# Optimization experiments

Measured on AMD Instinct MI355X. Metric: run time of the kernel, lower is better.

The kernel has to match this reference:

```python
import jax, jax.numpy as jnp
import numpy as np

B, G, NB, NC = 1024, 28, 2, 20
THR_CONF = 3.0
THR_NMS = 0.3
K = 4096            # fixed top-k detection slots (jit-friendly padding)
NEG = jnp.float32(-1e30)


def setup_inputs() -> dict:
    key = jax.random.key(0)
    k1, k2, k3 = jax.random.split(key, 3)
    return {
        "p_boxes": jax.random.normal(k1, (B, G, G, NB * 4), dtype=jnp.float32),
        "p_confs": jax.random.normal(k2, (B, G, G, NB), dtype=jnp.float32),
        "p_clses": jax.random.normal(k3, (B, G, G, NC), dtype=jnp.float32),
    }


def _decode_topk(p_boxes, p_confs, p_clses):
    # boxes: (B,G,G,NB,4) with (offx, offy, w, h) per box slot
    boxes = p_boxes.reshape(B, G, G, NB, 4)
    col = jnp.arange(G, dtype=jnp.float32)
    row = jnp.arange(G, dtype=jnp.float32)
    # offxy2xy: xy = (offxy + colrow) / num_grid  (dim1=row, dim2=col per torch.where order)
    cx = (boxes[..., 0] + col[None, None, :, None]) / G
    cy = (boxes[..., 1] + row[None, :, None, None]) / G
    w, h = boxes[..., 2], boxes[..., 3]
    # xywh2ltrb
    ltrb = jnp.stack([cx - w * 0.5, cy - h * 0.5, cx + w * 0.5, cy + h * 0.5], axis=-1)
    # label = argmax over classes + 1, shared by both box slots of a cell
    labels = jnp.argmax(p_clses, axis=-1) + 1                       # (B,G,G)
    labels = jnp.broadcast_to(labels[..., None], (B, G, G, NB))
    bids = jnp.broadcast_to(jnp.arange(B)[:, None, None, None], (B, G, G, NB))
    valid = p_confs > THR_CONF

    N = B * G * G * NB
    scores_masked = jnp.where(valid, p_confs, NEG).reshape(N)
    topv, topi = jax.lax.top_k(scores_masked, K)                    # sorted desc
    boxes_k = ltrb.reshape(N, 4)[topi]
    labels_k = labels.reshape(N)[topi]
    bids_k = bids.reshape(N)[topi]
    scores_k = p_confs.reshape(N)[topi]
    valid_k = topv > THR_CONF
    return bids_k, boxes_k, labels_k, scores_k, valid_k


def _iou_matrix(b):
    # b: (K,4) ltrb -> (K,K) pairwise IoU
    lt = jnp.maximum(b[:, None, :2], b[None, :, :2])
    rb = jnp.minimum(b[:, None, 2:], b[None, :, 2:])
    wh = jnp.clip(rb - lt, 0.0)
    inter = wh[..., 0] * wh[..., 1]
    area = jnp.clip(b[:, 2] - b[:, 0], 0.0) * jnp.clip(b[:, 3] - b[:, 1], 0.0)
    union = area[:, None] + area[None, :] - inter
    return inter / jnp.maximum(union, 1e-9)


def _nms(boxes, groups, valid):
    # per-(batch,label) NMS via group equality mask; boxes pre-sorted by score desc
    same = groups[:, None] == groups[None, :]
    suppress = same & (_iou_matrix(boxes) > THR_NMS)                # (K,K)
    idx = jnp.arange(K)

    def body(i, keep):
        sup = jnp.any(keep & suppress[:, i] & (idx < i))
        return keep.at[i].set(valid[i] & ~sup)

    return jax.lax.fori_loop(0, K, body, jnp.zeros((K,), dtype=bool))


def reference(p_boxes, p_confs, p_clses):
    bids, boxes, labels, scores, valid = _decode_topk(p_boxes, p_confs, p_clses)
    groups = bids * (NC + 1) + labels
    keep = _nms(boxes, groups, valid)
    # padded outputs of fixed size K; `keep` marks surviving detections
    return bids, boxes, labels, scores, keep
```

## Files before the change

### kernel.cpp

```cpp
#include <hip/hip_runtime.h>
#include <stdint.h>

#define B_    1024
#define G_    28
#define NB_   2
#define NC_   20
#define KK    4096
#define NTOT  (B_*G_*G_*NB_)
#define THRC  3.0f
#define THRN  0.3f
#define SORT_N 8192
#define NGRP  (B_*(NC_+1))
#define GCAP  8
#define RB    256
#define KPB   64
#define NRBF  (SORT_N/KPB)
#define CPT   16

#define WS_CNT   0
#define WS_GCNT  256
#define WS_ZERO_BYTES (256 + NGRP*4)
#define WS_KEYS  86272
#define WS_GMEM  (WS_KEYS + SORT_N*8)

typedef unsigned long long u64;

__global__ void k_zero(int4* __restrict__ p) {
    int t = blockIdx.x * blockDim.x + threadIdx.x;
    if (t < WS_ZERO_BYTES / 16) p[t] = make_int4(0, 0, 0, 0);
}

__global__ void k_collect(const float4* __restrict__ conf4, const float* __restrict__ clses,
                          u64* __restrict__ keys, int* cnt,
                          int* __restrict__ gcnt, u64* __restrict__ gmem) {
    int t = blockIdx.x * blockDim.x + threadIdx.x;
    int lane = threadIdx.x & 63;
    float cc[CPT];
    #pragma unroll
    for (int q = 0; q < CPT / 4; ++q) {
        float4 v = conf4[t * (CPT / 4) + q];
        cc[q * 4 + 0] = v.x; cc[q * 4 + 1] = v.y;
        cc[q * 4 + 2] = v.z; cc[q * 4 + 3] = v.w;
    }
    int nh = 0;
    #pragma unroll
    for (int u = 0; u < CPT; ++u) nh += (cc[u] > THRC);
    u64 act = __ballot(nh > 0);
    if (act) {
        int incl = nh;
        #pragma unroll
        for (int off = 1; off < 64; off <<= 1) {
            int v = __shfl_up(incl, off);
            if (lane >= off) incl += v;
        }
        int tot = __shfl(incl, 63);
        int base = 0;
        if (lane == 0) base = atomicAdd(cnt, tot);
        base = __shfl(base, 0);
        int pos = base + incl - nh;
        int fb = t * CPT;
        #pragma unroll
        for (int u = 0; u < CPT; ++u) {
            if (cc[u] > THRC) {
                int idx = fb + u;
                unsigned b = __float_as_uint(cc[u]);
                b = (b & 0x80000000u) ? ~b : (b | 0x80000000u);
                u64 key = ((u64)b << 32) | (u64)(0xFFFFFFFFu - (unsigned)idx);
                if (pos < SORT_N) keys[pos] = key;
                pos++;
                int cell = idx >> 1;
                const float4* cp4 = (const float4*)(clses + (size_t)cell * NC_);
                float best = -3.4e38f; int lab = 0;
                #pragma unroll
                for (int q = 0; q < 5; ++q) {
                    float4 cv = cp4[q];
                    float vv[4] = {cv.x, cv.y, cv.z, cv.w};
                    #pragma unroll
                    for (int w = 0; w < 4; ++w) {
                        int ci = q * 4 + w;
                        if (vv[w] > best) { best = vv[w]; lab = ci; }
                    }
                }
                int g = (cell / (G_ * G_)) * (NC_ + 1) + (lab + 1);
                int p2 = atomicAdd(&gcnt[g], 1);
                if (p2 < GCAP) gmem[(size_t)g * GCAP + p2] = key;
            }
        }
    }
}

__device__ inline float4 box_of(int idx, const float* __restrict__ boxes) {
    int nb = idx & 1;
    int cell = idx >> 1;
    int gx = cell % G_;
    int gy = (cell / G_) % G_;
    float4 bv = *(const float4*)(boxes + (size_t)cell * (NB_ * 4) + nb * 4);
    float cx = (bv.x + (float)gx) / (float)G_;
    float cy = (bv.y + (float)gy) / (float)G_;
    return make_float4(cx - bv.z * 0.5f, cy - bv.w * 0.5f,
                       cx + bv.z * 0.5f, cy + bv.w * 0.5f);
}

struct Dec { int b; int lab; };
__device__ inline Dec decode_write(int slot, int idx, float score,
                                   const float* __restrict__ boxes,
                                   const float* __restrict__ clses,
                                   float* __restrict__ out) {
    int cell = idx >> 1;
    int b = cell / (G_ * G_);
    float4 lt = box_of(idx, boxes);
    const float4* cp4 = (const float4*)(clses + (size_t)cell * NC_);
    float best = -3.4e38f; int lab = 0;
    #pragma unroll
    for (int q = 0; q < 5; ++q) {
        float4 cv = cp4[q];
        float vv[4] = {cv.x, cv.y, cv.z, cv.w};
        #pragma unroll
        for (int u = 0; u < 4; ++u) {
            int ci = q * 4 + u;
            if (vv[u] > best) { best = vv[u]; lab = ci; }
        }
    }
    lab += 1;
    out[slot] = (float)b;
    *(float4*)(out + KK + 4*slot) = lt;
    out[5*KK + slot] = (float)lab;
    out[6*KK + slot] = score;
    out[7*KK + slot] = 0.0f;
    Dec d; d.b = b; d.lab = lab;
    return d;
}

__global__ void __launch_bounds__(RB) k_rankdec(const float* __restrict__ boxes,
                                                const float4* __restrict__ conf4,
                                                const float* __restrict__ conf,
                                                const float* __restrict__ clses,
                                                const int* __restrict__ cnt,
                                                const u64* __restrict__ keys,
                                                float* __restrict__ out,
                                                const int* __restrict__ gcnt,
                                                const u64* __restrict__ gmem) {
    int tid = threadIdx.x;
    int lane = tid & 63;
    int Vtot = min(cnt[0], SORT_N);
    int V = min(Vtot, KK);

    if (blockIdx.x == NRBF) {
        __shared__ int wsum[4];
        int M = KK - V;
        if (M <= 0) return;
        unsigned mask = 0;
        int base = tid * 32;
        #pragma unroll
        for (int q = 0; q < 8; ++q) {
            float4 cv = conf4[tid * 8 + q];
            mask |= (unsigned)(!(cv.x > THRC)) << (q * 4 + 0);
            mask |= (unsigned)(!(cv.y > THRC)) << (q * 4 + 1);
            mask |= (unsigned)(!(cv.z > THRC)) << (q * 4 + 2);
            mask |= (unsigned)(!(cv.w > THRC)) << (q * 4 + 3);
        }
        int c = __popc(mask);
        int incl = c;
        #pragma unroll
        for (int off = 1; off < 64; off <<= 1) {
            int v = __shfl_up(incl, off);
            if (lane >= off) incl += v;
        }
        int wid = tid >> 6;
        if (lane == 63) wsum[wid] = incl;
        __syncthreads();
        int wbase = 0;
        for (int w = 0; w < wid; ++w) wbase += wsum[w];
        int p = wbase + incl - c;
        unsigned m = mask;
        while (m) {
            int u = __builtin_ctz(m);
            if (p < M) {
                int idx = base + u;
                decode_write(V + p, idx, conf[idx], boxes, clses, out);
            }
            p++;
            m &= m - 1;
        }
        return;
    }

    __shared__ u64 sk[SORT_N];
    __shared__ int partial[KPB][5];
    if (blockIdx.x * KPB >= Vtot) return;
    const ulonglong2* keys2 = (const ulonglong2*)keys;
    for (int i = tid; i * 2 < Vtot; i += RB) {
        ulonglong2 kv = keys2[i];
        sk[2 * i]     = kv.x;
        sk[2 * i + 1] = kv.y;
    }
    __syncthreads();

    int k = tid & (KPB - 1);
    int q = tid >> 6;
    int t = blockIdx.x * KPB + k;
    int chunk = (Vtot + 3) >> 2;
    int j0 = q * chunk;
    int j1 = min(j0 + chunk, Vtot);
    int r4 = 0;
    if (t < Vtot) {
        u64 k0 = sk[t];
        int j = j0;
        int lim = j0 + ((j1 - j0) & ~7);
        for (; j < lim; j += 8) {
            r4 += (int)(sk[j+0] > k0) + (int)(sk[j+1] > k0)
                + (int)(sk[j+2] > k0) + (int)(sk[j+3] > k0)
                + (int)(sk[j+4] > k0) + (int)(sk[j+5] > k0)
                + (int)(sk[j+6] > k0) + (int)(sk[j+7] > k0);
        }
        for (; j < j1; ++j) r4 += (int)(sk[j] > k0);
    }
    partial[k][q] = r4;
    __syncthreads();

    if (tid >= KPB || t >= Vtot) return;
    int r = partial[tid][0] + partial[tid][1] + partial[tid][2] + partial[tid][3];
    if (r >= KK) return;
    u64 k0 = sk[t];
    int idx = (int)(0xFFFFFFFFu - (unsigned)(k0 & 0xFFFFFFFFull));
    float score = __uint_as_float((unsigned)(k0 >> 32) ^ 0x80000000u);
    Dec d = decode_write(r, idx, score, boxes, clses, out);

    int g = d.b * (NC_ + 1) + d.lab;
    int m = min(gcnt[g], GCAP);
    u64 mem[GCAP];
    for (int i = 0; i < m; ++i) mem[i] = gmem[(size_t)g * GCAP + i];
    for (int i = 1; i < m; ++i) {
        u64 v = mem[i]; int qq = i - 1;
        while (qq >= 0 && mem[qq] < v) { mem[qq + 1] = mem[qq]; --qq; }
        mem[qq + 1] = v;
    }
    bool survive;
    if (m <= 1) {
        survive = true;
    } else {
        int own = 0;
        float4 bx[GCAP]; float ar[GCAP];
        for (int i = 0; i < m; ++i) {
            if (mem[i] == k0) own = i;
            int mi = (int)(0xFFFFFFFFu - (unsigned)(mem[i] & 0xFFFFFFFFull));
            bx[i] = box_of(mi, boxes);
            ar[i] = fmaxf(bx[i].z - bx[i].x, 0.f) * fmaxf(bx[i].w - bx[i].y, 0.f);
        }
        unsigned keepm = 0;
        for (int i = 0; i < m; ++i) {
            bool sup = false;
            for (int qq = 0; qq < i; ++qq) {
                if ((keepm >> qq) & 1u) {
                    float lx = fmaxf(bx[i].x, bx[qq].x), ly = fmaxf(bx[i].y, bx[qq].y);
                    float rx = fminf(bx[i].z, bx[qq].z), ry = fminf(bx[i].w, bx[qq].w);
                    float inter = fmaxf(rx - lx, 0.f) * fmaxf(ry - ly, 0.f);
                    float uni = ar[i] + ar[qq] - inter;
                    if (inter / fmaxf(uni, 1e-9f) > THRN) sup = true;
                }
            }
            if (!sup) keepm |= 1u << i;
        }
        survive = (keepm >> own) & 1u;
    }
    if (survive) out[7*KK + r] = 1.0f;
}

extern "C" void kernel_launch(void* const* d_in, const int* in_sizes, int n_in,
                              void* d_out, int out_size, void* d_ws, size_t ws_size,
                              hipStream_t stream) {
    const float* p_boxes = (const float*)d_in[0];
    const float* p_confs = (const float*)d_in[1];
    const float* p_clses = (const float*)d_in[2];
    float* out = (float*)d_out;
    char* ws = (char*)d_ws;

    int*  cnt   = (int*) (ws + WS_CNT);
    int*  gcnt  = (int*) (ws + WS_GCNT);
    u64*  keys  = (u64*) (ws + WS_KEYS);
    u64*  gmem  = (u64*) (ws + WS_GMEM);

    k_zero   <<<(WS_ZERO_BYTES / 16 + 255) / 256, 256, 0, stream>>>((int4*)ws);
    k_collect<<<NTOT / CPT / 256, 256, 0, stream>>>((const float4*)p_confs, p_clses,
                                                    keys, cnt, gcnt, gmem);
    k_rankdec<<<NRBF + 1, RB, 0, stream>>>(p_boxes, (const float4*)p_confs, p_confs,
                                           p_clses, cnt, keys, out, gcnt, gmem);
}
```

Baseline: 48.14 us.

## Find NMS group members during rank scan instead of global group buckets

Result: slower. 75.86 us (+57.6%).

```diff
diff --git a/kernel.cpp b/kernel.cpp
--- a/kernel.cpp
+++ b/kernel.cpp
@@ -7,32 +7,25 @@
 #define NC_   20
 #define KK    4096
 #define NTOT  (B_*G_*G_*NB_)
+#define IPB   (G_*G_*NB_)
 #define THRC  3.0f
 #define THRN  0.3f
 #define SORT_N 8192
-#define NGRP  (B_*(NC_+1))
 #define GCAP  8
+#define CAND_CAP 16
 #define RB    256
 #define KPB   64
 #define NRBF  (SORT_N/KPB)
 #define CPT   16
 
 #define WS_CNT   0
-#define WS_GCNT  256
-#define WS_ZERO_BYTES (256 + NGRP*4)
-#define WS_KEYS  86272
-#define WS_GMEM  (WS_KEYS + SORT_N*8)
+#define WS_KEYS  256
 
 typedef unsigned long long u64;
-
-__global__ void k_zero(int4* __restrict__ p) {
-    int t = blockIdx.x * blockDim.x + threadIdx.x;
-    if (t < WS_ZERO_BYTES / 16) p[t] = make_int4(0, 0, 0, 0);
-}
-
-__global__ void k_collect(const float4* __restrict__ conf4, const float* __restrict__ clses,
-                          u64* __restrict__ keys, int* cnt,
-                          int* __restrict__ gcnt, u64* __restrict__ gmem) {
+typedef unsigned short u16;
+
+__global__ void k_collect(const float4* __restrict__ conf4,
+                          u64* __restrict__ keys, int* cnt) {
     int t = blockIdx.x * blockDim.x + threadIdx.x;
     int lane = threadIdx.x & 63;
     float cc[CPT];
@@ -62,28 +55,12 @@
         #pragma unroll
         for (int u = 0; u < CPT; ++u) {
             if (cc[u] > THRC) {
-                int idx = fb + u;
-                unsigned b = __float_as_uint(cc[u]);
-                b = (b & 0x80000000u) ? ~b : (b | 0x80000000u);
-                u64 key = ((u64)b << 32) | (u64)(0xFFFFFFFFu - (unsigned)idx);
-                if (pos < SORT_N) keys[pos] = key;
+                if (pos < SORT_N) {
+                    unsigned b = __float_as_uint(cc[u]);
+                    b = (b & 0x80000000u) ? ~b : (b | 0x80000000u);
+                    keys[pos] = ((u64)b << 32) | (u64)(0xFFFFFFFFu - (unsigned)(fb + u));
+                }
                 pos++;
-                int cell = idx >> 1;
-                const float4* cp4 = (const float4*)(clses + (size_t)cell * NC_);
-                float best = -3.4e38f; int lab = 0;
-                #pragma unroll
-                for (int q = 0; q < 5; ++q) {
-                    float4 cv = cp4[q];
-                    float vv[4] = {cv.x, cv.y, cv.z, cv.w};
-                    #pragma unroll
-                    for (int w = 0; w < 4; ++w) {
-                        int ci = q * 4 + w;
-                        if (vv[w] > best) { best = vv[w]; lab = ci; }
-                    }
-                }
-                int g = (cell / (G_ * G_)) * (NC_ + 1) + (lab + 1);
-                int p2 = atomicAdd(&gcnt[g], 1);
-                if (p2 < GCAP) gmem[(size_t)g * GCAP + p2] = key;
             }
         }
     }
@@ -101,6 +78,22 @@
                        cx + bv.z * 0.5f, cy + bv.w * 0.5f);
 }
 
+__device__ inline int argmax20(const float* __restrict__ clses, int cell) {
+    const float4* cp4 = (const float4*)(clses + (size_t)cell * NC_);
+    float best = -3.4e38f; int lab = 0;
+    #pragma unroll
+    for (int q = 0; q < 5; ++q) {
+        float4 cv = cp4[q];
+        float vv[4] = {cv.x, cv.y, cv.z, cv.w};
+        #pragma unroll
+        for (int u = 0; u < 4; ++u) {
+            int ci = q * 4 + u;
+            if (vv[u] > best) { best = vv[u]; lab = ci; }
+        }
+    }
+    return lab;
+}
+
 struct Dec { int b; int lab; };
 __device__ inline Dec decode_write(int slot, int idx, float score,
                                    const float* __restrict__ boxes,
@@ -109,19 +102,7 @@
     int cell = idx >> 1;
     int b = cell / (G_ * G_);
     float4 lt = box_of(idx, boxes);
-    const float4* cp4 = (const float4*)(clses + (size_t)cell * NC_);
-    float best = -3.4e38f; int lab = 0;
-    #pragma unroll
-    for (int q = 0; q < 5; ++q) {
-        float4 cv = cp4[q];
-        float vv[4] = {cv.x, cv.y, cv.z, cv.w};
-        #pragma unroll
-        for (int u = 0; u < 4; ++u) {
-            int ci = q * 4 + u;
-            if (vv[u] > best) { best = vv[u]; lab = ci; }
-        }
-    }
-    lab += 1;
+    int lab = argmax20(clses, cell) + 1;
     out[slot] = (float)b;
     *(float4*)(out + KK + 4*slot) = lt;
     out[5*KK + slot] = (float)lab;
@@ -137,9 +118,7 @@
                                                 const float* __restrict__ clses,
                                                 const int* __restrict__ cnt,
                                                 const u64* __restrict__ keys,
-                                                float* __restrict__ out,
-                                                const int* __restrict__ gcnt,
-                                                const u64* __restrict__ gmem) {
+                                                float* __restrict__ out) {
     int tid = threadIdx.x;
     int lane = tid & 63;
     int Vtot = min(cnt[0], SORT_N);
@@ -187,7 +166,10 @@
 
     __shared__ u64 sk[SORT_N];
     __shared__ int partial[KPB][5];
+    __shared__ u16 cand[KPB][CAND_CAP];
+    __shared__ int ccnt[KPB];
     if (blockIdx.x * KPB >= Vtot) return;
+    if (tid < KPB) ccnt[tid] = 0;
     const ulonglong2* keys2 = (const ulonglong2*)keys;
     for (int i = tid; i * 2 < Vtot; i += RB) {
         ulonglong2 kv = keys2[i];
@@ -205,15 +187,19 @@
     int r4 = 0;
     if (t < Vtot) {
         u64 k0 = sk[t];
-        int j = j0;
-        int lim = j0 + ((j1 - j0) & ~7);
-        for (; j < lim; j += 8) {
-            r4 += (int)(sk[j+0] > k0) + (int)(sk[j+1] > k0)
-                + (int)(sk[j+2] > k0) + (int)(sk[j+3] > k0)
-                + (int)(sk[j+4] > k0) + (int)(sk[j+5] > k0)
-                + (int)(sk[j+6] > k0) + (int)(sk[j+7] > k0);
-        }
-        for (; j < j1; ++j) r4 += (int)(sk[j] > k0);
+        unsigned idx0 = 0xFFFFFFFFu - (unsigned)(k0 & 0xFFFFFFFFull);
+        unsigned b0 = idx0 / IPB;
+        unsigned H = 0xFFFFFFFFu - b0 * IPB;
+        unsigned L = H - (IPB - 1);
+        for (int j = j0; j < j1; ++j) {
+            u64 kj = sk[j];
+            r4 += (int)(kj > k0);
+            unsigned l32 = (unsigned)(kj & 0xFFFFFFFFull);
+            if (l32 >= L && l32 <= H) {
+                int p = atomicAdd(&ccnt[k], 1);
+                if (p < CAND_CAP) cand[k][p] = (u16)j;
+            }
+        }
     }
     partial[k][q] = r4;
     __syncthreads();
@@ -226,29 +212,35 @@
     float score = __uint_as_float((unsigned)(k0 >> 32) ^ 0x80000000u);
     Dec d = decode_write(r, idx, score, boxes, clses, out);
 
-    int g = d.b * (NC_ + 1) + d.lab;
-    int m = min(gcnt[g], GCAP);
+    int mc = min(ccnt[tid], CAND_CAP);
     u64 mem[GCAP];
-    for (int i = 0; i < m; ++i) mem[i] = gmem[(size_t)g * GCAP + i];
-    for (int i = 1; i < m; ++i) {
-        u64 v = mem[i]; int qq = i - 1;
-        while (qq >= 0 && mem[qq] < v) { mem[qq + 1] = mem[qq]; --qq; }
-        mem[qq + 1] = v;
+    int nm = 0;
+    for (int i = 0; i < mc; ++i) {
+        int j = cand[tid][i];
+        u64 kj = sk[j];
+        int idxj = (int)(0xFFFFFFFFu - (unsigned)(kj & 0xFFFFFFFFull));
+        int labj = argmax20(clses, idxj >> 1) + 1;
+        if (labj == d.lab && nm < GCAP) mem[nm++] = kj;
     }
     bool survive;
-    if (m <= 1) {
+    if (nm <= 1) {
         survive = true;
     } else {
+        for (int i = 1; i < nm; ++i) {
+            u64 v = mem[i]; int qq = i - 1;
+            while (qq >= 0 && mem[qq] < v) { mem[qq + 1] = mem[qq]; --qq; }
+            mem[qq + 1] = v;
+        }
         int own = 0;
         float4 bx[GCAP]; float ar[GCAP];
-        for (int i = 0; i < m; ++i) {
+        for (int i = 0; i < nm; ++i) {
             if (mem[i] == k0) own = i;
             int mi = (int)(0xFFFFFFFFu - (unsigned)(mem[i] & 0xFFFFFFFFull));
             bx[i] = box_of(mi, boxes);
             ar[i] = fmaxf(bx[i].z - bx[i].x, 0.f) * fmaxf(bx[i].w - bx[i].y, 0.f);
         }
         unsigned keepm = 0;
-        for (int i = 0; i < m; ++i) {
+        for (int i = 0; i < nm; ++i) {
             bool sup = false;
             for (int qq = 0; qq < i; ++qq) {
                 if ((keepm >> qq) & 1u) {
@@ -276,13 +268,10 @@
     char* ws = (char*)d_ws;
 
     int*  cnt   = (int*) (ws + WS_CNT);
-    int*  gcnt  = (int*) (ws + WS_GCNT);
     u64*  keys  = (u64*) (ws + WS_KEYS);
-    u64*  gmem  = (u64*) (ws + WS_GMEM);
-
-    k_zero   <<<(WS_ZERO_BYTES / 16 + 255) / 256, 256, 0, stream>>>((int4*)ws);
-    k_collect<<<NTOT / CPT / 256, 256, 0, stream>>>((const float4*)p_confs, p_clses,
-                                                    keys, cnt, gcnt, gmem);
+
+    hipMemsetAsync(cnt, 0, 4, stream);
+    k_collect<<<NTOT / CPT / 256, 256, 0, stream>>>((const float4*)p_confs, keys, cnt);
     k_rankdec<<<NRBF + 1, RB, 0, stream>>>(p_boxes, (const float4*)p_confs, p_confs,
-                                           p_clses, cnt, keys, out, gcnt, gmem);
-}
+                                           p_clses, cnt, keys, out);
+}
```
